# Optimization experiments

Measured on AMD Instinct MI355X. Metric: run time of the kernel, lower is better.

## Reference

```python
import jax, jax.numpy as jnp
import numpy as np

E = 2      # expansion
G = 8      # groups
K = 128    # num_clusters
N = 1024   # feature_size (dim)
D = E * N // G  # per-group cluster dim = 256
EPS = 1e-12


def _l2norm(v, axis):
    return v / jnp.maximum(jnp.linalg.norm(v, axis=axis, keepdims=True), EPS)


def setup_inputs() -> dict:
    key = jax.random.key(0)
    ks = jax.random.split(key, 8)
    x = jax.random.normal(ks[0], (64, N, 8, 8), dtype=jnp.float32)
    W_inp = jax.random.normal(ks[1], (E * N, N), dtype=jnp.float32) * 0.02
    b_inp = jax.random.uniform(ks[2], (E * N,), dtype=jnp.float32)
    W_g = jax.random.normal(ks[3], (G, E * N), dtype=jnp.float32) * 0.02
    b_g = jax.random.uniform(ks[4], (G,), dtype=jnp.float32)
    W_gk = jax.random.normal(ks[5], (G * K, E * N), dtype=jnp.float32) * 0.02
    b_gk = jax.random.uniform(ks[6], (G * K,), dtype=jnp.float32)
    centroids = jax.random.normal(ks[7], (K, D), dtype=jnp.float32) * 0.1
    return {"x": x, "W_inp": W_inp, "b_inp": b_inp, "W_g": W_g, "b_g": b_g,
            "W_gk": W_gk, "b_gk": b_gk, "centroids": centroids}


def reference(x, W_inp, b_inp, W_g, b_g, W_gk, b_gk, centroids):
    b8, c, h, w = x.shape
    bs = b8 // 8
    # [bs*8, C, H, W] -> [bs, M=8*H*W, N=C]
    x = x.reshape(bs, 8, c, h, w).transpose(0, 2, 1, 3, 4).reshape(bs, c, 8 * h * w)
    x = jnp.transpose(x, (0, 2, 1))            # [bs, M, N]
    M = x.shape[1]
    x = _l2norm(x, axis=2)                     # normalize_input
    x = x @ W_inp.T + b_inp                    # [bs, M, E*N]
    alpha_g = jax.nn.sigmoid(x @ W_g.T + b_g)  # [bs, M, G]
    # NOTE: original uses Softmax(dim=1) -> softmax over token dim M
    alpha_gk = jax.nn.softmax(x @ W_gk.T + b_gk, axis=1)   # [bs, M, G*K]
    alpha_gk = alpha_gk.reshape(bs, M, G, K)
    xr = x.reshape(bs, M, G, D)
    w_full = alpha_g[..., None] * alpha_gk     # [bs, M, G, K]
    # vlad[b,k,d] = sum_{m,g} w*(x - c) = einsum(w,x) - (sum w) * c
    vlad = jnp.einsum('bmgk,bmgd->bkd', w_full, xr) \
        - jnp.sum(w_full, axis=(1, 2))[..., None] * centroids  # [bs, K, D]
    vlad = _l2norm(vlad, axis=-1).reshape(bs, K * D)
    return _l2norm(vlad, axis=1)
```

## Files before the change

### kernel.cpp

```cpp
#include <hip/hip_runtime.h>
#include <hip/hip_bf16.h>
#include <math.h>

#define EPSN 1e-12f
typedef unsigned short ushort_t;

typedef float f32x4 __attribute__((ext_vector_type(4)));
typedef short s16x8 __attribute__((ext_vector_type(8)));
typedef unsigned short u16x8 __attribute__((ext_vector_type(8)));
typedef unsigned short u16x4 __attribute__((ext_vector_type(4)));

__device__ __forceinline__ void gload_lds16(const void* g, void* l) {
  __builtin_amdgcn_global_load_lds((const __attribute__((address_space(1))) void*)g,
                                   (__attribute__((address_space(3))) void*)l, 16, 0, 0);
}

__global__ void k0_ssq(const float* __restrict__ x, float* __restrict__ ssq8) {
  int b8 = blockIdx.x >> 3;
  int cc = blockIdx.x & 7;
  int t = threadIdx.x;
  int s4 = (t & 15) * 4;
  int cg = t >> 4;
  const float* xp = x + (size_t)b8 * 65536 + (size_t)cc * 128 * 64;
  float4 a = {0.f, 0.f, 0.f, 0.f};
#pragma unroll
  for (int j = 0; j < 8; ++j) {
    int c = cg + j * 16;
    float4 v = *(const float4*)(xp + (size_t)c * 64 + s4);
    a.x = fmaf(v.x, v.x, a.x);
    a.y = fmaf(v.y, v.y, a.y);
    a.z = fmaf(v.z, v.z, a.z);
    a.w = fmaf(v.w, v.w, a.w);
  }
  __shared__ float red[16][68];
  *(float4*)&red[cg][s4] = a;
  __syncthreads();
  if (t < 64) {
    float s = 0.f;
#pragma unroll
    for (int g = 0; g < 16; ++g) s += red[g][t];
    ssq8[cc * 4096 + b8 * 64 + t] = s;
  }
}

__global__ void k1_transpose(const float* __restrict__ x, const float* __restrict__ ssq8,
                             __hip_bfloat16* __restrict__ xnb) {
  int ct = blockIdx.x;
  int b8 = blockIdx.y;
  int t = threadIdx.x;
  __shared__ float tile[64][65];
  __shared__ float ivs[64];
  if (t < 64) {
    float s = 0.f;
#pragma unroll
    for (int cc = 0; cc < 8; ++cc) s += ssq8[cc * 4096 + b8 * 64 + t];
    ivs[t] = rsqrtf(fmaxf(s, 1e-24f));
  }
  int s = t & 63, cq = t >> 6;
  const float* xp = x + (size_t)b8 * 65536 + (size_t)ct * 64 * 64;
#pragma unroll
  for (int r = 0; r < 16; ++r) {
    int cl = cq * 16 + r;
    tile[cl][s] = xp[cl * 64 + s];
  }
  __syncthreads();
  int cl = t & 63, sq = t >> 6;
#pragma unroll
  for (int r = 0; r < 16; ++r) {
    int smm = sq * 16 + r;
    int tm = b8 * 64 + smm;
    xnb[(size_t)tm * 1024 + ct * 64 + cl] = __float2bfloat16(tile[cl][smm] * ivs[smm]);
  }
}

__global__ void kpack2(const float* __restrict__ Wi, const float* __restrict__ Wgk,
                       const float* __restrict__ W_g, const float* __restrict__ b_inp,
                       const float* __restrict__ b_g, __hip_bfloat16* __restrict__ oWi,
                       __hip_bfloat16* __restrict__ oWx, ushort_t* __restrict__ oWibT,
                       float* __restrict__ bWg) {
  int bid = blockIdx.x;
  int t = threadIdx.x;
  if (bid < 2048) {
    int i = (bid * 256 + t) * 4;
    float4 v = *(const float4*)(Wi + i);
    oWi[i + 0] = __float2bfloat16(v.x);
    oWi[i + 1] = __float2bfloat16(v.y);
    oWi[i + 2] = __float2bfloat16(v.z);
    oWi[i + 3] = __float2bfloat16(v.w);
  } else if (bid < 4096) {
    int i = ((bid - 2048) * 256 + t) * 4;
    float4 v = *(const float4*)(Wgk + i);
    oWx[i + 0] = __float2bfloat16(v.x);
    oWx[i + 1] = __float2bfloat16(v.y);
    oWx[i + 2] = __float2bfloat16(v.z);
    oWx[i + 3] = __float2bfloat16(v.w);
  } else if (bid < 4112) {
    int i = (bid - 4096) * 1024 + t * 4;
    float4 v = *(const float4*)(W_g + i);
    __hip_bfloat16* o = oWx + 1024 * 2048 + i;
    o[0] = __float2bfloat16(v.x);
    o[1] = __float2bfloat16(v.y);
    o[2] = __float2bfloat16(v.z);
    o[3] = __float2bfloat16(v.w);
  } else if (bid < 4352) {
    int i = (bid - 4112) * 1024 + t * 4;
    ushort_t* o = (ushort_t*)(oWx + 1032 * 2048) + i;
    *(u16x4*)o = (u16x4){0, 0, 0, 0};
  } else if (bid < 4360) {
    int j = bid - 4352;
    const float* row = W_g + (size_t)j * 2048;
    float s = 0.f;
    for (int c = t; c < 2048; c += 256) s = fmaf(b_inp[c], row[c], s);
    __shared__ float red[256];
    red[t] = s;
    __syncthreads();
    for (int o = 128; o > 0; o >>= 1) {
      if (t < o) red[t] += red[t + o];
      __syncthreads();
    }
    if (t == 0) bWg[j] = red[0] + b_g[j];
  } else if (bid < 4872) {
    int tt = bid - 4360;
    int cp0 = (tt >> 4) * 64;
    int c0 = (tt & 15) * 64;
    __shared__ ushort_t tile[64][72];
    int r = t >> 2, cs = (t & 3) * 16;
    const float* src = Wi + (size_t)(cp0 + r) * 1024 + c0 + cs;
#pragma unroll
    for (int j = 0; j < 16; j += 4) {
      float4 v = *(const float4*)(src + j);
      __hip_bfloat16 h0 = __float2bfloat16(v.x), h1 = __float2bfloat16(v.y);
      __hip_bfloat16 h2 = __float2bfloat16(v.z), h3 = __float2bfloat16(v.w);
      tile[r][cs + j + 0] = *(ushort_t*)&h0;
      tile[r][cs + j + 1] = *(ushort_t*)&h1;
      tile[r][cs + j + 2] = *(ushort_t*)&h2;
      tile[r][cs + j + 3] = *(ushort_t*)&h3;
    }
    __syncthreads();
    int c = t >> 2, ms = (t & 3) * 16;
    u16x8 o0, o1;
#pragma unroll
    for (int j = 0; j < 8; ++j) o0[j] = tile[ms + j][c];
#pragma unroll
    for (int j = 0; j < 8; ++j) o1[j] = tile[ms + 8 + j][c];
    ushort_t* dst = oWibT + (size_t)(c0 + c) * 2048 + cp0 + ms;
    *(u16x8*)dst = o0;
    *(u16x8*)(dst + 8) = o1;
  } else {
    int i = (bid - 4872) * 1024 + t * 4;
    ushort_t* o = (ushort_t*)oWi + (size_t)3200 * 1024 + i;
    *(u16x4*)o = (u16x4){0, 0, 0, 0};
  }
}

__launch_bounds__(512, 4)
__global__ void gemm0_splitk(const ushort_t* __restrict__ A, const ushort_t* __restrict__ B,
                             float* __restrict__ Cf) {
  const int Kstride = 2048, N = 1024;
  __shared__ alignas(16) ushort_t SH[32768];
  const int tid = threadIdx.x;
  const int m0 = blockIdx.y * 128, n0 = blockIdx.x * 128;
  const int s = blockIdx.z;
  const int koff = s * 512;
  const int w = tid >> 6, l = tid & 63;
  const int wr = w >> 2, wc = w & 3;
  const int srow = w * 8 + (l >> 3);
  const int ksw = ((l & 7) ^ (l >> 3)) * 8;
  const ushort_t* Ag0 = A + (size_t)(m0 + srow) * Kstride + ksw + koff;
  const ushort_t* Ag1 = A + (size_t)(m0 + 64 + srow) * Kstride + ksw + koff;
  const ushort_t* Bg0 = B + (size_t)(n0 + srow) * Kstride + ksw + koff;
  const ushort_t* Bg1 = B + (size_t)(n0 + 64 + srow) * Kstride + ksw + koff;
  const int l0 = w * 512;
  const int l1 = 4096 + w * 512;

  f32x4 acc[4][2];
#pragma unroll
  for (int i = 0; i < 4; ++i)
#pragma unroll
    for (int j = 0; j < 2; ++j) acc[i][j] = (f32x4){0.f, 0.f, 0.f, 0.f};

  const int sw = l & 7, qq = l >> 4;

#define ASH(buf) (SH + (buf)*8192)
#define BSH(buf) (SH + 16384 + (buf)*8192)
#define STAGE(buf, k0)                               \
  {                                                  \
    gload_lds16(Ag0 + (k0), ASH(buf) + l0);          \
    gload_lds16(Ag1 + (k0), ASH(buf) + l1);          \
    gload_lds16(Bg0 + (k0), BSH(buf) + l0);          \
    gload_lds16(Bg1 + (k0), BSH(buf) + l1);          \
  }
#define COMPUTE(buf)                                                                     \
  {                                                                                      \
    s16x8 af[4][2], bf[2][2];                                                            \
    _Pragma("unroll") for (int kk = 0; kk < 2; ++kk) {                                   \
      int slot = (((kk << 2) + qq) ^ sw) * 8;                                            \
      _Pragma("unroll") for (int mi = 0; mi < 4; ++mi)                                   \
          af[mi][kk] = *(const s16x8*)&ASH(buf)[(wr * 64 + mi * 16 + (l & 15)) * 64 +    \
                                               slot];                                   \
      _Pragma("unroll") for (int ni = 0; ni < 2; ++ni)                                   \
          bf[ni][kk] = *(const s16x8*)&BSH(buf)[(wc * 32 + ni * 16 + (l & 15)) * 64 +    \
                                               slot];                                   \
    }                                                                                    \
    _Pragma("unroll") for (int kk = 0; kk < 2; ++kk)                                     \
        _Pragma("unroll") for (int mi = 0; mi < 4; ++mi)                                 \
            _Pragma("unroll") for (int ni = 0; ni < 2; ++ni)                             \
                acc[mi][ni] = __builtin_amdgcn_mfma_f32_16x16x32_bf16(af[mi][kk],        \
                                                                     bf[ni][kk],        \
                                                                     acc[mi][ni], 0, 0, 0); \
  }

  STAGE(0, 0);
  int buf = 0;
  for (int t = 0; t < 7; ++t) {
    STAGE(buf ^ 1, (t + 1) << 6);
    asm volatile("s_waitcnt vmcnt(4)" ::: "memory");
    __builtin_amdgcn_s_barrier();
    asm volatile("" ::: "memory");
    COMPUTE(buf);
    asm volatile("" ::: "memory");
    __builtin_amdgcn_s_barrier();
    buf ^= 1;
  }
  asm volatile("s_waitcnt vmcnt(0)" ::: "memory");
  __builtin_amdgcn_s_barrier();
  asm volatile("" ::: "memory");
  COMPUTE(buf);
#undef STAGE
#undef COMPUTE
#undef ASH
#undef BSH

  float* Co = Cf + (size_t)s * 1152 * 1024;
#pragma unroll
  for (int mi = 0; mi < 4; ++mi) {
    int row = m0 + wr * 64 + mi * 16 + (l >> 4) * 4;
#pragma unroll
    for (int ni = 0; ni < 2; ++ni) {
      int col = n0 + wc * 32 + ni * 16 + (l & 15);
#pragma unroll
      for (int r = 0; r < 4; ++r)
        Co[(size_t)(row + r) * N + col] = acc[mi][ni][r];
    }
  }
}

__global__ void kpackC(const float* __restrict__ Wc4, ushort_t* __restrict__ dst) {
  int i = (blockIdx.x * 256 + threadIdx.x) * 4;
  float4 a = *(const float4*)(Wc4 + i);
  float4 b = *(const float4*)(Wc4 + 1179648 + i);
  float4 c = *(const float4*)(Wc4 + 2359296 + i);
  float4 d = *(const float4*)(Wc4 + 3538944 + i);
  float4 sv = {a.x + b.x + c.x + d.x, a.y + b.y + c.y + d.y,
               a.z + b.z + c.z + d.z, a.w + b.w + c.w + d.w};
  u16x4 o;
  __hip_bfloat16 h0 = __float2bfloat16(sv.x), h1 = __float2bfloat16(sv.y);
  __hip_bfloat16 h2 = __float2bfloat16(sv.z), h3 = __float2bfloat16(sv.w);
  o[0] = *(ushort_t*)&h0; o[1] = *(ushort_t*)&h1;
  o[2] = *(ushort_t*)&h2; o[3] = *(ushort_t*)&h3;
  *(u16x4*)(dst + i) = o;
}

__launch_bounds__(512, 2)
__global__ void gemm256_8ph(const ushort_t* __restrict__ A, const ushort_t* __restrict__ B,
                            ushort_t* __restrict__ C, int K, int N) {
  __shared__ alignas(16) ushort_t SH[65536];
  const int tid = threadIdx.x;
  const int m0 = blockIdx.y * 256, n0 = blockIdx.x * 256;
  const int w = tid >> 6, l = tid & 63;
  const int wr = w >> 2, wc = w & 3;
  const int r16 = l & 15, qq = l >> 4, sw = l & 7;
  const int s = tid >> 3;
  const int s_hi = s >> 5, s_lo = s & 31;
  const int ksw = ((tid & 7) ^ (s & 7)) * 8;
  const int NT = K >> 6;

  const ushort_t* pA0 = A + (size_t)(m0 + s) * K + ksw;
  const ushort_t* pA1 = A + (size_t)(m0 + 128 + s) * K + ksw;
  const ushort_t* pB0 = B + (size_t)(n0 + s_hi * 64 + s_lo) * K + ksw;
  const ushort_t* pB1 = B + (size_t)(n0 + 128 + s_hi * 64 + s_lo) * K + ksw;
  ushort_t* dA = SH + tid * 8;
  ushort_t* dB = SH + 32768 + tid * 8;

  f32x4 acc[8][4];
#pragma unroll
  for (int i = 0; i < 8; ++i)
#pragma unroll
    for (int j = 0; j < 4; ++j) acc[i][j] = (f32x4){0.f, 0.f, 0.f, 0.f};

#define SA(kt, h)                                                                        \
  {                                                                                      \
    gload_lds16(pA0 + (size_t)(h) * (K << 6) + ((kt) << 6),                              \
                dA + (((kt)&1) << 14) + ((h) << 13));                                    \
    gload_lds16(pA1 + (size_t)(h) * (K << 6) + ((kt) << 6),                              \
                dA + (((kt)&1) << 14) + ((h) << 13) + 4096);                             \
  }
#define SB(kt, h)                                                                        \
  {                                                                                      \
    gload_lds16(pB0 + (size_t)(h) * (K << 5) + ((kt) << 6),                              \
                dB + (((kt)&1) << 14) + ((h) << 13));                                    \
    gload_lds16(pB1 + (size_t)(h) * (K << 5) + ((kt) << 6),                              \
                dB + (((kt)&1) << 14) + ((h) << 13) + 4096);                             \
  }
#define VMC4 asm volatile("s_waitcnt vmcnt(4)" ::: "memory")

#define PHASE(d, mh, nh, STG, VM)                                                        \
  {                                                                                      \
    s16x8 af[2][4], bf[2][2];                                                            \
    _Pragma("unroll") for (int kk = 0; kk < 2; ++kk) {                                   \
      int slot = (((kk << 2) + qq) ^ sw) * 8;                                            \
      _Pragma("unroll") for (int ni2 = 0; ni2 < 2; ++ni2)                                \
          bf[kk][ni2] = *(const s16x8*)&SH[32768 + ((d) << 14) + ((nh) << 13) +          \
                                           (wc * 32 + ni2 * 16 + r16) * 64 + slot];      \
      _Pragma("unroll") for (int mi2 = 0; mi2 < 4; ++mi2)                                \
          af[kk][mi2] = *(const s16x8*)&SH[((d) << 14) + ((mh) << 13) +                  \
                                           (wr * 64 + mi2 * 16 + r16) * 64 + slot];      \
    }                                                                                    \
    STG;                                                                                 \
    asm volatile("" ::: "memory");                                                       \
    __builtin_amdgcn_s_barrier();                                                        \
    asm volatile("" ::: "memory");                                                       \
    __builtin_amdgcn_s_setprio(1);                                                       \
    _Pragma("unroll") for (int kk = 0; kk < 2; ++kk)                                     \
        _Pragma("unroll") for (int mi2 = 0; mi2 < 4; ++mi2)                              \
            _Pragma("unroll") for (int ni2 = 0; ni2 < 2; ++ni2)                          \
                acc[(mh)*4 + mi2][(nh)*2 + ni2] = __builtin_amdgcn_mfma_f32_16x16x32_bf16( \
                    af[kk][mi2], bf[kk][ni2], acc[(mh)*4 + mi2][(nh)*2 + ni2], 0, 0, 0); \
    __builtin_amdgcn_s_setprio(0);                                                       \
    VM;                                                                                  \
    asm volatile("" ::: "memory");                                                       \
    __builtin_amdgcn_s_barrier();                                                        \
    asm volatile("" ::: "memory");                                                       \
  }

  SA(0, 0); SB(0, 0); SA(0, 1); SB(0, 1); SA(1, 0); SB(1, 0);
  VMC4;
  __builtin_amdgcn_s_barrier();
  asm volatile("" ::: "memory");

#pragma unroll 1
  for (int I = 0; I < (NT >> 1); ++I) {
    const int kt = 2 * I;
    const int k1 = kt + 1, k2 = kt + 2, k3 = kt + 3;
    PHASE(0, 0, 0, SA(k1, 1), );
    PHASE(0, 0, 1, SB(k1, 1), );
    PHASE(0, 1, 0, if (k2 < NT) SA(k2, 0), );
    PHASE(0, 1, 1, if (k2 < NT) SB(k2, 0), VMC4);
    PHASE(1, 0, 0, if (k2 < NT) SA(k2, 1), );
    PHASE(1, 0, 1, if (k2 < NT) SB(k2, 1), );
    PHASE(1, 1, 0, if (k3 < NT) SA(k3, 0), );
    PHASE(1, 1, 1, if (k3 < NT) SB(k3, 0), VMC4);
  }
#undef PHASE
#undef SA
#undef SB
#undef VMC4

#pragma unroll
  for (int mi = 0; mi < 8; ++mi) {
    int row = m0 + wr * 128 + mi * 16 + (l >> 4) * 4;
#pragma unroll
    for (int ni = 0; ni < 4; ++ni) {
      int col = n0 + wc * 64 + ni * 16 + r16;
#pragma unroll
      for (int r = 0; r < 4; ++r) {
        __hip_bfloat16 hb = __float2bfloat16(acc[mi][ni][r]);
        C[(size_t)(row + r) * N + col] = *(ushort_t*)&hb;
      }
    }
  }
}

__launch_bounds__(256)
__global__ void k5_softmax(const ushort_t* __restrict__ logitsTb, const float* __restrict__ bWg,
                           float* __restrict__ colsumW, ushort_t* __restrict__ wbT) {
  int wv = (blockIdx.x << 2) + (threadIdx.x >> 6);
  int q = wv >> 3, b = wv & 7;
  int l = threadIdx.x & 63;
  int g = q >> 7;
  size_t base = (size_t)q * 4096 + b * 512 + l * 8;
  u16x8 v8 = *(const u16x8*)(logitsTb + base);
  float vs[8];
#pragma unroll
  for (int i = 0; i < 8; ++i) vs[i] = __uint_as_float(((unsigned)v8[i]) << 16);
  float M = vs[0];
#pragma unroll
  for (int i = 1; i < 8; ++i) M = fmaxf(M, vs[i]);
#pragma unroll
  for (int m = 1; m < 64; m <<= 1) M = fmaxf(M, __shfl_xor(M, m, 64));
  float e[8], S = 0.f;
#pragma unroll
  for (int i = 0; i < 8; ++i) {
    e[i] = expf(vs[i] - M);
    S += e[i];
  }
#pragma unroll
  for (int m = 1; m < 64; m <<= 1) S += __shfl_xor(S, m, 64);
  float R = 1.0f / S;
  u16x8 g8 = *(const u16x8*)(logitsTb + (size_t)(1024 + g) * 4096 + b * 512 + l * 8);
  float bg = bWg[g];
  float wv8[8], wsum = 0.f;
#pragma unroll
  for (int i = 0; i < 8; ++i) {
    float gl = __uint_as_float(((unsigned)g8[i]) << 16);
    float ag = 1.0f / (1.0f + expf(-(gl + bg)));
    wv8[i] = e[i] * R * ag;
    wsum += wv8[i];
  }
#pragma unroll
  for (int m = 1; m < 64; m <<= 1) wsum += __shfl_xor(wsum, m, 64);
  if (l == 0) colsumW[b * 1024 + q] = wsum;
  u16x8 o;
#pragma unroll
  for (int i = 0; i < 8; ++i) {
    __hip_bfloat16 hb = __float2bfloat16(wv8[i]);
    o[i] = *(ushort_t*)&hb;
  }
  *(u16x8*)(wbT + base) = o;
}

__launch_bounds__(256)
__global__ void k6_vlad_mfma(const ushort_t* __restrict__ wbT, const ushort_t* __restrict__ YcT,
                             float* __restrict__ vpart) {
  int kt = blockIdx.x >> 2, dt = blockIdx.x & 3;
  int ms = blockIdx.y, b = blockIdx.z;
  __shared__ alignas(16) ushort_t Ash[2][4096];
  __shared__ alignas(16) ushort_t Bsh[2][4096];
  const int tid = threadIdx.x;
  const int w = tid >> 6, l = tid & 63;
  const int wr = w >> 1, wc = w & 1;
  const int crow = l >> 3;
  const int ksw = ((l & 7) ^ crow) * 8;

  const ushort_t* Ap[2];
  const ushort_t* Bp[2];
  int loff[2];
#pragma unroll
  for (int c = 0; c < 2; ++c) {
    int chunk = w * 2 + c;
    Ap[c] = wbT + (size_t)(kt * 64 + chunk * 8 + crow) * 4096 + b * 512 + ms * 64 + ksw;
    Bp[c] = YcT + (size_t)(dt * 64 + chunk * 8 + crow) * 4096 + b * 512 + ms * 64 + ksw;
    loff[c] = chunk * 512;
  }

  f32x4 acc[2][2];
#pragma unroll
  for (int i = 0; i < 2; ++i)
#pragma unroll
    for (int j = 0; j < 2; ++j) acc[i][j] = (f32x4){0.f, 0.f, 0.f, 0.f};

  const int sw = l & 7, qq = l >> 4;

#define STAGE6(buf, g)                                                       \
  {                                                                          \
    size_t offA = (size_t)(g)*524288;                                        \
    size_t offB = (size_t)(g)*1048576;                                       \
    gload_lds16(Ap[0] + offA, &Ash[buf][loff[0]]);                           \
    gload_lds16(Ap[1] + offA, &Ash[buf][loff[1]]);                           \
    gload_lds16(Bp[0] + offB, &Bsh[buf][loff[0]]);                           \
    gload_lds16(Bp[1] + offB, &Bsh[buf][loff[1]]);                           \
  }
#define COMPUTE6(buf)                                                                    \
  {                                                                                      \
    s16x8 af[2][2], bf[2][2];                                                            \
    _Pragma("unroll") for (int kk = 0; kk < 2; ++kk) {                                   \
      int slot = (((kk << 2) + qq) ^ sw) * 8;                                            \
      _Pragma("unroll") for (int mi = 0; mi < 2; ++mi) {                                 \
        af[mi][kk] = *(const s16x8*)&Ash[buf][(wr * 32 + mi * 16 + (l & 15)) * 64 +      \
                                             slot];                                     \
        bf[mi][kk] = *(const s16x8*)&Bsh[buf][(wc * 32 + mi * 16 + (l & 15)) * 64 +      \
                                             slot];                                     \
      }                                                                                  \
    }                                                                                    \
    _Pragma("unroll") for (int kk = 0; kk < 2; ++kk)                                     \
        _Pragma("unroll") for (int mi = 0; mi < 2; ++mi)                                 \
            _Pragma("unroll") for (int ni = 0; ni < 2; ++ni)                             \
                acc[mi][ni] = __builtin_amdgcn_mfma_f32_16x16x32_bf16(af[mi][kk],        \
                                                                     bf[ni][kk],        \
                                                                     acc[mi][ni], 0, 0, 0); \
  }

  STAGE6(0, 0);
  int buf = 0;
  for (int s = 0; s < 7; ++s) {
    STAGE6(buf ^ 1, s + 1);
    asm volatile("s_waitcnt vmcnt(4)" ::: "memory");
    __builtin_amdgcn_s_barrier();
    asm volatile("" ::: "memory");
    COMPUTE6(buf);
    asm volatile("" ::: "memory");
    __builtin_amdgcn_s_barrier();
    buf ^= 1;
  }
  asm volatile("s_waitcnt vmcnt(0)" ::: "memory");
  __builtin_amdgcn_s_barrier();
  asm volatile("" ::: "memory");
  COMPUTE6(buf);
#undef STAGE6
#undef COMPUTE6

#pragma unroll
  for (int mi = 0; mi < 2; ++mi) {
    int row = kt * 64 + wr * 32 + mi * 16 + (l >> 4) * 4;
#pragma unroll
    for (int ni = 0; ni < 2; ++ni) {
      int col = dt * 64 + wc * 32 + ni * 16 + (l & 15);
#pragma unroll
      for (int r = 0; r < 4; ++r)
        vpart[((size_t)(ms * 8 + b) * 128 + row + r) * 256 + col] = acc[mi][ni][r];
    }
  }
}

__global__ void k7_intranorm(const float* __restrict__ vpart, const float* __restrict__ colsumW,
                             const float* __restrict__ b_inp, const float* __restrict__ cent,
                             float* __restrict__ out, float* __restrict__ ss1) {
  int k = blockIdx.x;
  int b = blockIdx.y;
  int d = threadIdx.x;
  float S = 0.f, bp = 0.f;
#pragma unroll
  for (int g = 0; g < 8; ++g) {
    float cw = colsumW[b * 1024 + g * 128 + k];
    S += cw;
    bp = fmaf(b_inp[g * 256 + d], cw, bp);
  }
  size_t off = ((size_t)b * 128 + k) * 256 + d;
  float v = bp - S * cent[(size_t)k * 256 + d];
#pragma unroll
  for (int i = 0; i < 8; ++i) v += vpart[off + (size_t)i * 262144];
  float ss = v * v;
#pragma unroll
  for (int m = 1; m < 64; m <<= 1) ss += __shfl_xor(ss, m, 64);
  __shared__ float red[4];
  int lane = d & 63, wv = d >> 6;
  if (lane == 0) red[wv] = ss;
  __syncthreads();
  float tot = red[0] + red[1] + red[2] + red[3];
  float rinv = 1.0f / fmaxf(sqrtf(tot), EPSN);
  out[off] = v * rinv;
  if (d == 0) ss1[b * 128 + k] = tot * rinv * rinv;
}

__global__ void k8_finalnorm(const float* __restrict__ ss1, float* __restrict__ out) {
  int b = blockIdx.x;
  int t = threadIdx.x;
  __shared__ float red[256];
  red[t] = (t < 128) ? ss1[b * 128 + t] : 0.f;
  __syncthreads();
  for (int o = 128; o > 0; o >>= 1) {
    if (t < o) red[t] += red[t + o];
    __syncthreads();
  }
  float rinv = 1.0f / fmaxf(sqrtf(red[0]), EPSN);
  float* op = out + (size_t)b * 32768;
  for (int i = t; i < 32768; i += 256) op[i] *= rinv;
}

extern "C" void kernel_launch(void* const* d_in, const int* in_sizes, int n_in,
                              void* d_out, int out_size, void* d_ws, size_t ws_size,
                              hipStream_t stream) {
  const float* x     = (const float*)d_in[0];
  const float* W_inp = (const float*)d_in[1];
  const float* b_inp = (const float*)d_in[2];
  const float* W_g   = (const float*)d_in[3];
  const float* b_g   = (const float*)d_in[4];
  const float* W_gk  = (const float*)d_in[5];
  const float* cent  = (const float*)d_in[7];
  float* out = (float*)d_out;
  float* ws = (float*)d_ws;

  float* ssq8    = ws + 0;
  float* colsumW = ws + 32768;
  float* ss1     = ws + 40960;
  float* bWg     = ws + 41984;
  ushort_t* xnb  = (ushort_t*)(ws + 42048);
  ushort_t* wbT  = xnb;
  ushort_t* stackedA = (ushort_t*)(ws + 2139200);
  ushort_t* WibT = (ushort_t*)(ws + 3843136);
  ushort_t* Wgkx = (ushort_t*)(ws + 4891712);
  float* vpart   = ws + 3843136;
  float* Wc4     = ws + 6071360;
  ushort_t* Cstacked = (ushort_t*)(ws + 6071360);
  ushort_t* YcT      = Cstacked;
  ushort_t* logitsTb = Cstacked + (size_t)2048 * 4096;

  k0_ssq<<<512, 256, 0, stream>>>(x, ssq8);
  k1_transpose<<<dim3(16, 64), 256, 0, stream>>>(x, ssq8, (__hip_bfloat16*)xnb);
  kpack2<<<5000, 256, 0, stream>>>(W_inp, W_gk, W_g, b_inp, b_g,
                                   (__hip_bfloat16*)stackedA, (__hip_bfloat16*)Wgkx, WibT, bWg);
  gemm0_splitk<<<dim3(8, 9, 4), 512, 0, stream>>>(Wgkx, WibT, Wc4);
  kpackC<<<1152, 256, 0, stream>>>(Wc4, stackedA + (size_t)2048 * 1024);
  gemm256_8ph<<<dim3(16, 13), 512, 0, stream>>>(stackedA, xnb, Cstacked, 1024, 4096);
  k5_softmax<<<2048, 256, 0, stream>>>(logitsTb, bWg, colsumW, wbT);
  k6_vlad_mfma<<<dim3(8, 8, 8), 256, 0, stream>>>(wbT, YcT, vpart);
  k7_intranorm<<<dim3(128, 8), 256, 0, stream>>>(vpart, colsumW, b_inp, cent, out, ss1);
  k8_finalnorm<<<8, 256, 0, stream>>>(ss1, out);
}
```

Measured before the change: 122.9 us.

## Fuse ssq kernel into weight-pack launch and pair GEMM phases sharing A fragments

The standalone sum-of-squares kernel is merged into the kpack2 launch as extra blocks, which removes one kernel launch and lets that work run alongside the weight packing. In gemm256_8ph, the two phases that share the same A half now run as one paired phase. A fragments are loaded from LDS once and reused for both B halves, cutting redundant LDS reads. The risks are changed register pressure and a different schedule for barriers and staging.

New measurement: 117.0 us. 4.8% less time.

```diff
diff --git a/kernel.cpp b/kernel.cpp
--- a/kernel.cpp
+++ b/kernel.cpp
@@ -13,34 +13,6 @@
 __device__ __forceinline__ void gload_lds16(const void* g, void* l) {
   __builtin_amdgcn_global_load_lds((const __attribute__((address_space(1))) void*)g,
                                    (__attribute__((address_space(3))) void*)l, 16, 0, 0);
-}
-
-__global__ void k0_ssq(const float* __restrict__ x, float* __restrict__ ssq8) {
-  int b8 = blockIdx.x >> 3;
-  int cc = blockIdx.x & 7;
-  int t = threadIdx.x;
-  int s4 = (t & 15) * 4;
-  int cg = t >> 4;
-  const float* xp = x + (size_t)b8 * 65536 + (size_t)cc * 128 * 64;
-  float4 a = {0.f, 0.f, 0.f, 0.f};
-#pragma unroll
-  for (int j = 0; j < 8; ++j) {
-    int c = cg + j * 16;
-    float4 v = *(const float4*)(xp + (size_t)c * 64 + s4);
-    a.x = fmaf(v.x, v.x, a.x);
-    a.y = fmaf(v.y, v.y, a.y);
-    a.z = fmaf(v.z, v.z, a.z);
-    a.w = fmaf(v.w, v.w, a.w);
-  }
-  __shared__ float red[16][68];
-  *(float4*)&red[cg][s4] = a;
-  __syncthreads();
-  if (t < 64) {
-    float s = 0.f;
-#pragma unroll
-    for (int g = 0; g < 16; ++g) s += red[g][t];
-    ssq8[cc * 4096 + b8 * 64 + t] = s;
-  }
 }
 
 __global__ void k1_transpose(const float* __restrict__ x, const float* __restrict__ ssq8,
@@ -77,7 +49,8 @@
                        const float* __restrict__ W_g, const float* __restrict__ b_inp,
                        const float* __restrict__ b_g, __hip_bfloat16* __restrict__ oWi,
                        __hip_bfloat16* __restrict__ oWx, ushort_t* __restrict__ oWibT,
-                       float* __restrict__ bWg) {
+                       float* __restrict__ bWg, const float* __restrict__ x,
+                       float* __restrict__ ssq8) {
   int bid = blockIdx.x;
   int t = threadIdx.x;
   if (bid < 2048) {
@@ -146,10 +119,36 @@
     ushort_t* dst = oWibT + (size_t)(c0 + c) * 2048 + cp0 + ms;
     *(u16x8*)dst = o0;
     *(u16x8*)(dst + 8) = o1;
-  } else {
+  } else if (bid < 5000) {
     int i = (bid - 4872) * 1024 + t * 4;
     ushort_t* o = (ushort_t*)oWi + (size_t)3200 * 1024 + i;
     *(u16x4*)o = (u16x4){0, 0, 0, 0};
+  } else {
+    int kb = bid - 5000;
+    int b8 = kb >> 3;
+    int cc = kb & 7;
+    int s4 = (t & 15) * 4;
+    int cg = t >> 4;
+    const float* xp = x + (size_t)b8 * 65536 + (size_t)cc * 128 * 64;
+    float4 a = {0.f, 0.f, 0.f, 0.f};
+#pragma unroll
+    for (int j = 0; j < 8; ++j) {
+      int c = cg + j * 16;
+      float4 v = *(const float4*)(xp + (size_t)c * 64 + s4);
+      a.x = fmaf(v.x, v.x, a.x);
+      a.y = fmaf(v.y, v.y, a.y);
+      a.z = fmaf(v.z, v.z, a.z);
+      a.w = fmaf(v.w, v.w, a.w);
+    }
+    __shared__ float red0[16][68];
+    *(float4*)&red0[cg][s4] = a;
+    __syncthreads();
+    if (t < 64) {
+      float s = 0.f;
+#pragma unroll
+      for (int g = 0; g < 16; ++g) s += red0[g][t];
+      ssq8[cc * 4096 + b8 * 64 + t] = s;
+    }
   }
 }
 
@@ -304,19 +303,19 @@
   }
 #define VMC4 asm volatile("s_waitcnt vmcnt(4)" ::: "memory")
 
-#define PHASE(d, mh, nh, STG, VM)                                                        \
+#define PHASEPAIR(d, mh, STG1, VM1, STG2, VM2)                                           \
   {                                                                                      \
     s16x8 af[2][4], bf[2][2];                                                            \
     _Pragma("unroll") for (int kk = 0; kk < 2; ++kk) {                                   \
       int slot = (((kk << 2) + qq) ^ sw) * 8;                                            \
-      _Pragma("unroll") for (int ni2 = 0; ni2 < 2; ++ni2)                                \
-          bf[kk][ni2] = *(const s16x8*)&SH[32768 + ((d) << 14) + ((nh) << 13) +          \
-                                           (wc * 32 + ni2 * 16 + r16) * 64 + slot];      \
       _Pragma("unroll") for (int mi2 = 0; mi2 < 4; ++mi2)                                \
           af[kk][mi2] = *(const s16x8*)&SH[((d) << 14) + ((mh) << 13) +                  \
                                            (wr * 64 + mi2 * 16 + r16) * 64 + slot];      \
+      _Pragma("unroll") for (int ni2 = 0; ni2 < 2; ++ni2)                                \
+          bf[kk][ni2] = *(const s16x8*)&SH[32768 + ((d) << 14) +                         \
+                                           (wc * 32 + ni2 * 16 + r16) * 64 + slot];      \
     }                                                                                    \
-    STG;                                                                                 \
+    STG1;                                                                                \
     asm volatile("" ::: "memory");                                                       \
     __builtin_amdgcn_s_barrier();                                                        \
     asm volatile("" ::: "memory");                                                       \
@@ -324,10 +323,31 @@
     _Pragma("unroll") for (int kk = 0; kk < 2; ++kk)                                     \
         _Pragma("unroll") for (int mi2 = 0; mi2 < 4; ++mi2)                              \
             _Pragma("unroll") for (int ni2 = 0; ni2 < 2; ++ni2)                          \
-                acc[(mh)*4 + mi2][(nh)*2 + ni2] = __builtin_amdgcn_mfma_f32_16x16x32_bf16( \
-                    af[kk][mi2], bf[kk][ni2], acc[(mh)*4 + mi2][(nh)*2 + ni2], 0, 0, 0); \
+                acc[(mh)*4 + mi2][ni2] = __builtin_amdgcn_mfma_f32_16x16x32_bf16(        \
+                    af[kk][mi2], bf[kk][ni2], acc[(mh)*4 + mi2][ni2], 0, 0, 0);          \
     __builtin_amdgcn_s_setprio(0);                                                       \
-    VM;                                                                                  \
+    VM1;                                                                                 \
+    asm volatile("" ::: "memory");                                                       \
+    __builtin_amdgcn_s_barrier();                                                        \
+    asm volatile("" ::: "memory");                                                       \
+    _Pragma("unroll") for (int kk = 0; kk < 2; ++kk) {                                   \
+      int slot = (((kk << 2) + qq) ^ sw) * 8;                                            \
+      _Pragma("unroll") for (int ni2 = 0; ni2 < 2; ++ni2)                                \
+          bf[kk][ni2] = *(const s16x8*)&SH[32768 + ((d) << 14) + 8192 +                  \
+                                           (wc * 32 + ni2 * 16 + r16) * 64 + slot];      \
+    }                                                                                    \
+    STG2;                                                                                \
+    asm volatile("" ::: "memory");                                                       \
+    __builtin_amdgcn_s_barrier();                                                        \
+    asm volatile("" ::: "memory");                                                       \
+    __builtin_amdgcn_s_setprio(1);                                                       \
+    _Pragma("unroll") for (int kk = 0; kk < 2; ++kk)                                     \
+        _Pragma("unroll") for (int mi2 = 0; mi2 < 4; ++mi2)                              \
+            _Pragma("unroll") for (int ni2 = 0; ni2 < 2; ++ni2)                          \
+                acc[(mh)*4 + mi2][2 + ni2] = __builtin_amdgcn_mfma_f32_16x16x32_bf16(    \
+                    af[kk][mi2], bf[kk][ni2], acc[(mh)*4 + mi2][2 + ni2], 0, 0, 0);      \
+    __builtin_amdgcn_s_setprio(0);                                                       \
+    VM2;                                                                                 \
     asm volatile("" ::: "memory");                                                       \
     __builtin_amdgcn_s_barrier();                                                        \
     asm volatile("" ::: "memory");                                                       \
@@ -342,16 +362,12 @@
   for (int I = 0; I < (NT >> 1); ++I) {
     const int kt = 2 * I;
     const int k1 = kt + 1, k2 = kt + 2, k3 = kt + 3;
-    PHASE(0, 0, 0, SA(k1, 1), );
-    PHASE(0, 0, 1, SB(k1, 1), );
-    PHASE(0, 1, 0, if (k2 < NT) SA(k2, 0), );
-    PHASE(0, 1, 1, if (k2 < NT) SB(k2, 0), VMC4);
-    PHASE(1, 0, 0, if (k2 < NT) SA(k2, 1), );
-    PHASE(1, 0, 1, if (k2 < NT) SB(k2, 1), );
-    PHASE(1, 1, 0, if (k3 < NT) SA(k3, 0), );
-    PHASE(1, 1, 1, if (k3 < NT) SB(k3, 0), VMC4);
-  }
-#undef PHASE
+    PHASEPAIR(0, 0, SA(k1, 1), , SB(k1, 1), );
+    PHASEPAIR(0, 1, if (k2 < NT) SA(k2, 0), , if (k2 < NT) SB(k2, 0), VMC4);
+    PHASEPAIR(1, 0, if (k2 < NT) SA(k2, 1), , if (k2 < NT) SB(k2, 1), );
+    PHASEPAIR(1, 1, if (k3 < NT) SA(k3, 0), , if (k3 < NT) SB(k3, 0), VMC4);
+  }
+#undef PHASEPAIR
 #undef SA
 #undef SB
 #undef VMC4
@@ -585,10 +601,10 @@
   ushort_t* YcT      = Cstacked;
   ushort_t* logitsTb = Cstacked + (size_t)2048 * 4096;
 
-  k0_ssq<<<512, 256, 0, stream>>>(x, ssq8);
+  kpack2<<<5512, 256, 0, stream>>>(W_inp, W_gk, W_g, b_inp, b_g,
+                                   (__hip_bfloat16*)stackedA, (__hip_bfloat16*)Wgkx, WibT, bWg,
+                                   x, ssq8);
   k1_transpose<<<dim3(16, 64), 256, 0, stream>>>(x, ssq8, (__hip_bfloat16*)xnb);
-  kpack2<<<5000, 256, 0, stream>>>(W_inp, W_gk, W_g, b_inp, b_g,
-                                   (__hip_bfloat16*)stackedA, (__hip_bfloat16*)Wgkx, WibT, bWg);
   gemm0_splitk<<<dim3(8, 9, 4), 512, 0, stream>>>(Wgkx, WibT, Wc4);
   kpackC<<<1152, 256, 0, stream>>>(Wc4, stackedA + (size_t)2048 * 1024);
   gemm256_8ph<<<dim3(16, 13), 512, 0, stream>>>(stackedA, xnb, Cstacked, 1024, 4096);
```
